# Kernel optimization log

Measured on AMD Instinct MI355X. Metric: run time of the kernel, lower is better.

The kernel has to match this reference:

```python
import jax, jax.numpy as jnp
import numpy as np

N_NODES = 30000
NEG_SLOPE = 0.2  # PyG GATConv default leaky_relu slope


def gat_conv(x, src, dst, W, a_src, a_dst, b, num_nodes, concat):
    """One PyG-style GATConv layer (add_self_loops already applied to src/dst).
    x: [N, F_in]; W: [F_in, H*C]; a_src, a_dst: [H, C]; b: [H*C] or [C].
    """
    H, C = a_src.shape
    h = (x @ W).reshape(num_nodes, H, C)                     # [N, H, C]
    alpha_src = jnp.einsum('nhc,hc->nh', h, a_src)           # [N, H]
    alpha_dst = jnp.einsum('nhc,hc->nh', h, a_dst)           # [N, H]
    e = jax.nn.leaky_relu(alpha_src[src] + alpha_dst[dst], NEG_SLOPE)  # [E, H]
    # scatter-softmax over incoming edges of each dst node
    e_max = jax.ops.segment_max(e, dst, num_segments=num_nodes)        # [N, H]
    e_exp = jnp.exp(e - e_max[dst])                                    # [E, H]
    denom = jax.ops.segment_sum(e_exp, dst, num_segments=num_nodes)    # [N, H]
    alpha = e_exp / denom[dst]                                         # [E, H]
    msg = h[src] * alpha[:, :, None]                                   # [E, H, C]
    out = jax.ops.segment_sum(msg, dst, num_segments=num_nodes)        # [N, H, C]
    out = out.reshape(num_nodes, H * C) if concat else out.mean(axis=1)
    return out + b


def _glorot(key, shape):
    fan = sum(shape[:2]) if len(shape) > 1 else shape[0] * 2
    return jax.random.normal(key, shape, dtype=jnp.float32) * np.sqrt(2.0 / fan)


def setup_inputs() -> dict:
    key = jax.random.key(0)
    ks = jax.random.split(key, 16)
    n, f_in, heads = N_NODES, 256, 4
    x = jax.random.normal(ks[0], (n, f_in), dtype=jnp.float32)
    edge_index = jax.random.randint(ks[1], (2, 480000), 0, n, dtype=jnp.int64)
    inp = {
        'x': x, 'edge_index': edge_index,
        'W1': _glorot(ks[2], (f_in, heads * 128)),
        'a1s': _glorot(ks[3], (heads, 128)), 'a1d': _glorot(ks[4], (heads, 128)),
        'b1': jnp.zeros((heads * 128,), jnp.float32),
        'W2': _glorot(ks[5], (heads * 128, heads * 128)),
        'a2s': _glorot(ks[6], (heads, 128)), 'a2d': _glorot(ks[7], (heads, 128)),
        'b2': jnp.zeros((heads * 128,), jnp.float32),
        'W3': _glorot(ks[8], (heads * 128, heads * 64)),
        'a3s': _glorot(ks[9], (heads, 64)), 'a3d': _glorot(ks[10], (heads, 64)),
        'b3': jnp.zeros((heads * 64,), jnp.float32),
        # conv4: 256 -> 64, 1 head, mean (concat=False)
        'W4': _glorot(ks[11], (heads * 64, 64)),
        'a4s': _glorot(ks[12], (1, 64)), 'a4d': _glorot(ks[13], (1, 64)),
        'b4': jnp.zeros((64,), jnp.float32),
    }
    return inp


def reference(x, edge_index, W1, a1s, a1d, b1, W2, a2s, a2d, b2,
              W3, a3s, a3d, b3, W4, a4s, a4d, b4):
    n = x.shape[0]
    # PyG GATConv default add_self_loops=True
    loops = jnp.arange(n, dtype=edge_index.dtype)
    src = jnp.concatenate([edge_index[0], loops])
    dst = jnp.concatenate([edge_index[1], loops])
    h = jax.nn.relu(gat_conv(x, src, dst, W1, a1s, a1d, b1, n, True))
    h = jax.nn.relu(gat_conv(h, src, dst, W2, a2s, a2d, b2, n, True))
    h = jax.nn.relu(gat_conv(h, src, dst, W3, a3s, a3d, b3, n, True))
    h = jax.nn.relu(gat_conv(h, src, dst, W4, a4s, a4d, b4, n, False))
    return h
```

## Files before the change

kernel.cpp:

```cpp
#include <hip/hip_runtime.h>
#include <hip/hip_fp16.h>
#include <math.h>


typedef __attribute__((ext_vector_type(8))) __bf16 bf16x8;
typedef __attribute__((ext_vector_type(4))) float floatx4;
typedef __attribute__((ext_vector_type(8))) unsigned short usv8;
typedef __attribute__((ext_vector_type(4))) unsigned short usv4;

#define DEG_CAP 256

__device__ __forceinline__ unsigned short f2bf(float f) {
    unsigned int u = __float_as_uint(f);
    u += 0x7fff + ((u >> 16) & 1);
    return (unsigned short)(u >> 16);
}
__device__ __forceinline__ float bf2f(unsigned short u) {
    return __uint_as_float(((unsigned int)u) << 16);
}
__device__ __forceinline__ float lrelu(float e) {
    return (e > 0.f) ? e : 0.2f * e;
}
__device__ __forceinline__ void gload16(const void* g, void* l) {
    __builtin_amdgcn_global_load_lds(
        (const __attribute__((address_space(1))) void*)g,
        (__attribute__((address_space(3))) void*)l, 16, 0, 0);
}

static __global__ void zero_float(float* __restrict__ p, int n) {
    int i = blockIdx.x * blockDim.x + threadIdx.x;
    if (i < n) p[i] = 0.f;
}
static __global__ void zero_int(int* __restrict__ p, int n) {
    int i = blockIdx.x * blockDim.x + threadIdx.x;
    if (i < n) p[i] = 0;
}

static __global__ void hist_kernel(const int* __restrict__ ei, int e0, int n_nodes,
                                   int* __restrict__ counts) {
    int e = blockIdx.x * blockDim.x + threadIdx.x;
    int et = e0 + n_nodes;
    if (e >= et) return;
    int d = (e < e0) ? ei[e0 + e] : (e - e0);
    atomicAdd(&counts[d], 1);
}

static __global__ void scan_kernel(const int* __restrict__ counts,
                                   int* __restrict__ row_ptr,
                                   int* __restrict__ cursor, int n) {
    __shared__ int sdata[1024];
    int tid = threadIdx.x;
    int per = (n + 1023) / 1024;
    int start = tid * per;
    int stop = min(start + per, n);
    if (start > n) start = n;
    int s = 0;
    for (int i = start; i < stop; i++) s += counts[i];
    sdata[tid] = s;
    __syncthreads();
    for (int off = 1; off < 1024; off <<= 1) {
        int t = (tid >= off) ? sdata[tid - off] : 0;
        __syncthreads();
        sdata[tid] += t;
        __syncthreads();
    }
    int run = sdata[tid] - s;
    for (int i = start; i < stop; i++) {
        row_ptr[i] = run;
        cursor[i] = run;
        run += counts[i];
    }
    if (stop == n) row_ptr[n] = run;
}

static __global__ void scatter_kernel(const int* __restrict__ ei, int e0, int n_nodes,
                                      int* __restrict__ cursor,
                                      int* __restrict__ src_sorted) {
    int e = blockIdx.x * blockDim.x + threadIdx.x;
    int et = e0 + n_nodes;
    if (e >= et) return;
    int s, d;
    if (e < e0) { s = ei[e]; d = ei[e0 + e]; } else { s = e - e0; d = s; }
    int pos = atomicAdd(&cursor[d], 1);
    src_sorted[pos] = s;
}

static __global__ void convA_kernel(const float* __restrict__ X,
                                    unsigned short* __restrict__ A, int M, int K) {
    int idx = blockIdx.x * 256 + threadIdx.x;
    if (idx >= M * K) return;
    int m = idx / K, k = idx % K;
    float v = X[idx];
    unsigned short hi = f2bf(v);
    size_t base = (size_t)m * (2 * K);
    A[base + k] = hi;
    A[base + K + k] = f2bf(v - bf2f(hi));
}

__device__ __forceinline__ void convW_one(const float* W, unsigned short* BT,
                                          int idx, int K, int N) {
    int n = idx / K, k = idx % K;
    float v = (n < N) ? W[(size_t)k * N + n] : 0.f;
    unsigned short hi = f2bf(v);
    size_t base = (size_t)n * (2 * K);
    BT[base + k] = hi;
    BT[base + K + k] = f2bf(v - bf2f(hi));
}

static __global__ void convW_all(const float* __restrict__ W1, unsigned short* __restrict__ BT1,
                                 const float* __restrict__ W2, unsigned short* __restrict__ BT2,
                                 const float* __restrict__ W3, unsigned short* __restrict__ BT3,
                                 const float* __restrict__ W4, unsigned short* __restrict__ BT4) {
    int idx = blockIdx.x * 256 + threadIdx.x;
    if (idx < 131072) { convW_one(W1, BT1, idx, 256, 512); return; }
    idx -= 131072;
    if (idx < 262144) { convW_one(W2, BT2, idx, 512, 512); return; }
    idx -= 262144;
    if (idx < 131072) { convW_one(W3, BT3, idx, 512, 256); return; }
    idx -= 131072;
    if (idx < 32768)  { convW_one(W4, BT4, idx, 256, 64); }
}

#define BM 128
#define BN 128
#define BKK 32

__launch_bounds__(256, 3)
static __global__ void gemm_mfma(const unsigned short* __restrict__ A,
                                 const unsigned short* __restrict__ B,
                                 __half* __restrict__ C, int M, int K, int N,
                                 int xcols, int mblocks,
                                 const float* __restrict__ asv,
                                 const float* __restrict__ adv,
                                 float* __restrict__ as_out,
                                 float* __restrict__ ad_out,
                                 int Hh, int Cc) {
    __shared__ __align__(16) unsigned short lds[4 * BM * BKK];
    const int tid  = threadIdx.x;
    const int lane = tid & 63;
    const int wave = tid >> 6;

    const int id = blockIdx.x;
    const int band = id / (8 * xcols);
    const int rem = id - band * 8 * xcols;
    const int band_rows = min(8, mblocks - band * 8);
    const int ry = rem % band_rows;
    const int rx = rem / band_rows;
    const int r0 = (band * 8 + ry) * BM;
    const int c0 = rx * BN;

    const int wm = (wave >> 1) * 64;
    const int wn = (wave & 1) * 64;
    const int q   = lane >> 4;
    const int m16 = lane & 15;

    floatx4 acc[4][4];
#pragma unroll
    for (int i = 0; i < 4; i++)
#pragma unroll
        for (int j = 0; j < 4; j++) acc[i][j] = {0.f, 0.f, 0.f, 0.f};

    const size_t sA = (size_t)(2 * K);
    const size_t sB = (size_t)(2 * K);
    char* ldsb = (char*)lds;

#pragma unroll 1
    for (int k0 = 0; k0 < K; k0 += BKK) {
        __syncthreads();
#pragma unroll
        for (int c = 0; c < 2; c++) {
            int slot = c * 256 + tid;
            int row = slot >> 2;
            int gc  = (slot & 3) ^ ((row >> 1) & 3);
            const unsigned short* Ab = A + (size_t)(r0 + row) * sA + k0 + gc * 8;
            const unsigned short* Bb = B + (size_t)(c0 + row) * sB + k0 + gc * 8;
            gload16(Ab,     ldsb + slot * 16);
            gload16(Ab + K, ldsb + 8192 + slot * 16);
            gload16(Bb,     ldsb + 16384 + slot * 16);
            gload16(Bb + K, ldsb + 24576 + slot * 16);
        }
        __syncthreads();
        bf16x8 ah[4], al[4], bh[4], bl[4];
#pragma unroll
        for (int i = 0; i < 4; i++) {
            int row = wm + i * 16 + m16;
            int ch  = q ^ ((row >> 1) & 3);
            int off = (row * 4 + ch) * 16;
            ah[i] = *(const bf16x8*)(ldsb + off);
            al[i] = *(const bf16x8*)(ldsb + 8192 + off);
        }
#pragma unroll
        for (int j = 0; j < 4; j++) {
            int row = wn + j * 16 + m16;
            int ch  = q ^ ((row >> 1) & 3);
            int off = (row * 4 + ch) * 16;
            bh[j] = *(const bf16x8*)(ldsb + 16384 + off);
            bl[j] = *(const bf16x8*)(ldsb + 24576 + off);
        }
#pragma unroll
        for (int i = 0; i < 4; i++)
#pragma unroll
            for (int j = 0; j < 4; j++) {
                acc[i][j] = __builtin_amdgcn_mfma_f32_16x16x32_bf16(
                    ah[i], bh[j], acc[i][j], 0, 0, 0);
                acc[i][j] = __builtin_amdgcn_mfma_f32_16x16x32_bf16(
                    al[i], bh[j], acc[i][j], 0, 0, 0);
                acc[i][j] = __builtin_amdgcn_mfma_f32_16x16x32_bf16(
                    ah[i], bl[j], acc[i][j], 0, 0, 0);
            }
    }
#pragma unroll
    for (int i = 0; i < 4; i++)
#pragma unroll
        for (int j = 0; j < 4; j++)
#pragma unroll
            for (int r = 0; r < 4; r++) {
                int row = r0 + wm + i * 16 + q * 4 + r;
                int col = c0 + wn + j * 16 + m16;
                if (row < M && col < N)
                    C[(size_t)row * N + col] = __float2half(acc[i][j][r]);
            }
    if (c0 + wn < N) {
        int head = (c0 + wn) / Cc;
#pragma unroll
        for (int i = 0; i < 4; i++)
#pragma unroll
            for (int r = 0; r < 4; r++) {
                float ps = 0.f, pd = 0.f;
#pragma unroll
                for (int j = 0; j < 4; j++) {
                    int c = c0 + wn + j * 16 + m16;
                    float v = acc[i][j][r];
                    ps = fmaf(v, asv[c], ps);
                    pd = fmaf(v, adv[c], pd);
                }
#pragma unroll
                for (int off = 1; off < 16; off <<= 1) {
                    ps += __shfl_xor(ps, off);
                    pd += __shfl_xor(pd, off);
                }
                if (m16 == 0) {
                    int row = r0 + wm + i * 16 + q * 4 + r;
                    if (row < M) {
                        atomicAdd(&as_out[(size_t)row * Hh + head], ps);
                        atomicAdd(&ad_out[(size_t)row * Hh + head], pd);
                    }
                }
            }
    }
}

template <int R>
__device__ __forceinline__ void accum_row(const __half* hptr, size_t off, float w,
                                          float* acc) {
    const __half* p = hptr + off;
    if constexpr (R == 8) {
        float4 raw = *(const float4*)p;
        const __half* hv = (const __half*)&raw;
#pragma unroll
        for (int r = 0; r < 8; r++) acc[r] = fmaf(__half2float(hv[r]), w, acc[r]);
    } else if constexpr (R == 4) {
        float2 raw = *(const float2*)p;
        const __half* hv = (const __half*)&raw;
#pragma unroll
        for (int r = 0; r < 4; r++) acc[r] = fmaf(__half2float(hv[r]), w, acc[r]);
    } else {
        acc[0] = fmaf(__half2float(*p), w, acc[0]);
    }
}

template <int H, int C, bool BF16OUT>
__launch_bounds__(256)
static __global__ void agg_kernel(const __half* __restrict__ h,
                                  const float* __restrict__ as_arr,
                                  const float* __restrict__ ad_arr,
                                  const int* __restrict__ row_ptr,
                                  const int* __restrict__ src_sorted,
                                  const float* __restrict__ bias,
                                  float* __restrict__ outf,
                                  unsigned short* __restrict__ outb,
                                  float* __restrict__ znext_as,
                                  float* __restrict__ znext_ad, int n_nodes) {
    constexpr int R = H * C / 64;
    constexpr int G = 64 / H;
    constexpr int K = H * C;
    __shared__ float lds_e[4][DEG_CAP * H];
    int wave = threadIdx.x >> 6;
    int lane = threadIdx.x & 63;
    int n = blockIdx.x * 4 + wave;
    if (n >= n_nodes) return;
    int beg = row_ptr[n], end = row_ptr[n + 1];
    float* we = lds_e[wave];

    float ad_h[H], m_h[H], l_h[H];
#pragma unroll
    for (int hh = 0; hh < H; hh++) {
        ad_h[hh] = ad_arr[(size_t)n * H + hh];
        m_h[hh] = -INFINITY;
        l_h[hh] = 0.f;
    }
    for (int base = beg; base < end; base += 64) {
        int j = base + lane;
        bool ok = j < end;
        float e_h[H];
        if (ok) {
            int s = src_sorted[j];
            if constexpr (H == 4) {
                float4 a = ((const float4*)as_arr)[s];
                e_h[0] = lrelu(a.x + ad_h[0]);
                e_h[1] = lrelu(a.y + ad_h[1]);
                e_h[2] = lrelu(a.z + ad_h[2]);
                e_h[3] = lrelu(a.w + ad_h[3]);
            } else {
                e_h[0] = lrelu(as_arr[s] + ad_h[0]);
            }
            int idx = j - beg;
            if (idx < DEG_CAP) {
                if constexpr (H == 4) {
                    *(float4*)&we[idx * 4] = make_float4(e_h[0], e_h[1], e_h[2], e_h[3]);
                } else {
                    we[idx] = e_h[0];
                }
            }
        } else {
#pragma unroll
            for (int hh = 0; hh < H; hh++) e_h[hh] = -INFINITY;
        }
#pragma unroll
        for (int hh = 0; hh < H; hh++) {
            float cm = e_h[hh];
#pragma unroll
            for (int off = 1; off < 64; off <<= 1) cm = fmaxf(cm, __shfl_xor(cm, off));
            float newm = fmaxf(m_h[hh], cm);
            float p = ok ? __expf(e_h[hh] - newm) : 0.f;
#pragma unroll
            for (int off = 1; off < 64; off <<= 1) p += __shfl_xor(p, off);
            l_h[hh] = l_h[hh] * __expf(m_h[hh] - newm) + p;
            m_h[hh] = newm;
        }
    }
    int myh = lane / G;
    float mm, adm, inv;
    if constexpr (H == 4) {
        mm  = m_h[0];  mm  = (myh == 1) ? m_h[1] : mm;  mm  = (myh == 2) ? m_h[2] : mm;  mm  = (myh == 3) ? m_h[3] : mm;
        float ll = l_h[0]; ll = (myh == 1) ? l_h[1] : ll; ll = (myh == 2) ? l_h[2] : ll; ll = (myh == 3) ? l_h[3] : ll;
        adm = ad_h[0]; adm = (myh == 1) ? ad_h[1] : adm; adm = (myh == 2) ? ad_h[2] : adm; adm = (myh == 3) ? ad_h[3] : adm;
        inv = 1.f / ll;
    } else {
        mm = m_h[0]; adm = ad_h[0]; inv = 1.f / l_h[0];
    }

    float acc[R];
#pragma unroll
    for (int r = 0; r < R; r++) acc[r] = 0.f;

    int j = beg;
    for (; j + 3 < end; j += 4) {
        int i0 = j - beg;
        int s0 = src_sorted[j];
        int s1 = src_sorted[j + 1];
        int s2 = src_sorted[j + 2];
        int s3 = src_sorted[j + 3];
        float e0, e1, e2, e3;
        if (i0 + 3 < DEG_CAP) {
            e0 = we[(i0 + 0) * H + myh];
            e1 = we[(i0 + 1) * H + myh];
            e2 = we[(i0 + 2) * H + myh];
            e3 = we[(i0 + 3) * H + myh];
        } else {
            e0 = lrelu(as_arr[(size_t)s0 * H + myh] + adm);
            e1 = lrelu(as_arr[(size_t)s1 * H + myh] + adm);
            e2 = lrelu(as_arr[(size_t)s2 * H + myh] + adm);
            e3 = lrelu(as_arr[(size_t)s3 * H + myh] + adm);
        }
        float w0 = __expf(e0 - mm) * inv;
        float w1 = __expf(e1 - mm) * inv;
        float w2 = __expf(e2 - mm) * inv;
        float w3 = __expf(e3 - mm) * inv;
        accum_row<R>(h, (size_t)s0 * K + lane * R, w0, acc);
        accum_row<R>(h, (size_t)s1 * K + lane * R, w1, acc);
        accum_row<R>(h, (size_t)s2 * K + lane * R, w2, acc);
        accum_row<R>(h, (size_t)s3 * K + lane * R, w3, acc);
    }
    for (; j < end; j++) {
        int i0 = j - beg;
        int s0 = src_sorted[j];
        float e0 = (i0 < DEG_CAP) ? we[i0 * H + myh]
                                  : lrelu(as_arr[(size_t)s0 * H + myh] + adm);
        float w0 = __expf(e0 - mm) * inv;
        accum_row<R>(h, (size_t)s0 * K + lane * R, w0, acc);
    }

    if (znext_as != nullptr && lane == 0) {
        if constexpr (H == 4) {
            *(float4*)&znext_as[(size_t)n * 4] = make_float4(0.f, 0.f, 0.f, 0.f);
            *(float4*)&znext_ad[(size_t)n * 4] = make_float4(0.f, 0.f, 0.f, 0.f);
        } else {
            znext_as[n] = 0.f;
            znext_ad[n] = 0.f;
        }
    }
    float vout[R];
#pragma unroll
    for (int r = 0; r < R; r++)
        vout[r] = fmaxf(acc[r] + bias[lane * R + r], 0.f);

    if constexpr (BF16OUT) {
        unsigned short hi[R], lo[R];
#pragma unroll
        for (int r = 0; r < R; r++) {
            hi[r] = f2bf(vout[r]);
            lo[r] = f2bf(vout[r] - bf2f(hi[r]));
        }
        size_t base = (size_t)n * (2 * K) + lane * R;
        if constexpr (R == 8) {
            usv8 vh = {hi[0], hi[1], hi[2], hi[3], hi[4], hi[5], hi[6], hi[7]};
            usv8 vl = {lo[0], lo[1], lo[2], lo[3], lo[4], lo[5], lo[6], lo[7]};
            *(usv8*)(outb + base) = vh;
            *(usv8*)(outb + base + K) = vl;
        } else if constexpr (R == 4) {
            usv4 vh = {hi[0], hi[1], hi[2], hi[3]};
            usv4 vl = {lo[0], lo[1], lo[2], lo[3]};
            *(usv4*)(outb + base) = vh;
            *(usv4*)(outb + base + K) = vl;
        } else {
#pragma unroll
            for (int r = 0; r < R; r++) {
                outb[base + r] = hi[r];
                outb[base + K + r] = lo[r];
            }
        }
    } else {
#pragma unroll
        for (int r = 0; r < R; r++)
            outf[(size_t)n * K + lane * R + r] = vout[r];
    }
}


static inline size_t align_up(size_t x) { return (x + 255) & ~(size_t)255; }

extern "C" void kernel_launch(void* const* d_in, const int* in_sizes, int n_in,
                              void* d_out, int out_size, void* d_ws, size_t ws_size,
                              hipStream_t stream) {
    const float* x   = (const float*)d_in[0];
    const int*   ei  = (const int*)d_in[1];
    const float* W1  = (const float*)d_in[2];
    const float* a1s = (const float*)d_in[3];
    const float* a1d = (const float*)d_in[4];
    const float* b1  = (const float*)d_in[5];
    const float* W2  = (const float*)d_in[6];
    const float* a2s = (const float*)d_in[7];
    const float* a2d = (const float*)d_in[8];
    const float* b2  = (const float*)d_in[9];
    const float* W3  = (const float*)d_in[10];
    const float* a3s = (const float*)d_in[11];
    const float* a3d = (const float*)d_in[12];
    const float* b3  = (const float*)d_in[13];
    const float* W4  = (const float*)d_in[14];
    const float* a4s = (const float*)d_in[15];
    const float* a4d = (const float*)d_in[16];
    const float* b4  = (const float*)d_in[17];

    const int n  = in_sizes[0] / 256;
    const int e0 = in_sizes[1] / 2;
    const int et = e0 + n;
    const int Mpad = ((n + 127) / 128) * 128;

    char* w = (char*)d_ws;
    unsigned short* slotA = (unsigned short*)w;  w += align_up((size_t)Mpad * 1024 * 2);
    __half* hbuf = (__half*)w;                   w += align_up((size_t)n * 512 * 4);
    unsigned short* WT1 = (unsigned short*)w;    w += align_up((size_t)512 * 512 * 2);
    unsigned short* WT2 = (unsigned short*)w;    w += align_up((size_t)512 * 1024 * 2);
    unsigned short* WT3 = (unsigned short*)w;    w += align_up((size_t)256 * 1024 * 2);
    unsigned short* WT4 = (unsigned short*)w;    w += align_up((size_t)128 * 512 * 2);
    float* asA = (float*)w;                      w += align_up((size_t)n * 4 * 4);
    float* adA = (float*)w;                      w += align_up((size_t)n * 4 * 4);
    float* asB = (float*)w;                      w += align_up((size_t)n * 4 * 4);
    float* adB = (float*)w;                      w += align_up((size_t)n * 4 * 4);
    int* row_ptr = (int*)w;                      w += align_up((size_t)(n + 1) * 4);
    int* counts  = (int*)w;                      w += align_up((size_t)n * 4);
    int* cursor  = (int*)w;                      w += align_up((size_t)n * 4);
    int* src_sorted = (int*)w;                   w += align_up((size_t)et * 4);
    (void)ws_size;

    dim3 blk(256);
    int nodeblocks = (n + 3) / 4;

    zero_int<<<(n + 255) / 256, 256, 0, stream>>>(counts, n);
    hist_kernel<<<(et + 255) / 256, 256, 0, stream>>>(ei, e0, n, counts);
    scan_kernel<<<1, 1024, 0, stream>>>(counts, row_ptr, cursor, n);
    scatter_kernel<<<(et + 255) / 256, 256, 0, stream>>>(ei, e0, n, cursor, src_sorted);

    convA_kernel<<<((n * 256) + 255) / 256, blk, 0, stream>>>(x, slotA, n, 256);
    convW_all<<<(557056 + 255) / 256, blk, 0, stream>>>(W1, WT1, W2, WT2, W3, WT3, W4, WT4);
    zero_float<<<(n * 8 + 255) / 256, blk, 0, stream>>>(asA, n * 8);

    const int mblocks = Mpad / 128;

    gemm_mfma<<<dim3(4 * mblocks), blk, 0, stream>>>(slotA, WT1, hbuf, n, 256, 512, 4, mblocks,
                                                     a1s, a1d, asA, adA, 4, 128);
    agg_kernel<4, 128, true><<<nodeblocks, blk, 0, stream>>>(hbuf, asA, adA, row_ptr, src_sorted, b1, nullptr, slotA, asB, adB, n);

    gemm_mfma<<<dim3(4 * mblocks), blk, 0, stream>>>(slotA, WT2, hbuf, n, 512, 512, 4, mblocks,
                                                     a2s, a2d, asB, adB, 4, 128);
    agg_kernel<4, 128, true><<<nodeblocks, blk, 0, stream>>>(hbuf, asB, adB, row_ptr, src_sorted, b2, nullptr, slotA, asA, adA, n);

    gemm_mfma<<<dim3(2 * mblocks), blk, 0, stream>>>(slotA, WT3, hbuf, n, 512, 256, 2, mblocks,
                                                     a3s, a3d, asA, adA, 4, 64);
    agg_kernel<4, 64, true><<<nodeblocks, blk, 0, stream>>>(hbuf, asA, adA, row_ptr, src_sorted, b3, nullptr, slotA, asB, adB, n);

    gemm_mfma<<<dim3(1 * mblocks), blk, 0, stream>>>(slotA, WT4, hbuf, n, 256, 64, 1, mblocks,
                                                     a4s, a4d, asB, adB, 1, 64);
    agg_kernel<1, 64, false><<<nodeblocks, blk, 0, stream>>>(hbuf, asB, adB, row_ptr, src_sorted, b4, (float*)d_out, nullptr, nullptr, nullptr, n);
}
```

Measured before the change: 639.6 us.

## Switch GEMM operands from split-bf16 to fp16 activations with split-fp16 weights

Activations are now stored as a single fp16 value instead of a bf16 hi/lo pair, and weights as an fp16 hi/lo pair. Each tile product therefore needs two MFMA calls instead of three, and the activation loads, LDS footprint and aggregation output writes are halved. Activations are double-buffered in separate fp16 buffers. The risk is lower accuracy: fp16 activations carry about 11 bits of mantissa and have limited range, where split bf16 carried about 16 bits.

```diff
diff --git a/kernel.cpp b/kernel.cpp
--- a/kernel.cpp
+++ b/kernel.cpp
@@ -3,21 +3,13 @@
 #include <math.h>
 
 
-typedef __attribute__((ext_vector_type(8))) __bf16 bf16x8;
+typedef __attribute__((ext_vector_type(8))) _Float16 f16x8;
 typedef __attribute__((ext_vector_type(4))) float floatx4;
 typedef __attribute__((ext_vector_type(8))) unsigned short usv8;
 typedef __attribute__((ext_vector_type(4))) unsigned short usv4;
 
 #define DEG_CAP 256
 
-__device__ __forceinline__ unsigned short f2bf(float f) {
-    unsigned int u = __float_as_uint(f);
-    u += 0x7fff + ((u >> 16) & 1);
-    return (unsigned short)(u >> 16);
-}
-__device__ __forceinline__ float bf2f(unsigned short u) {
-    return __uint_as_float(((unsigned int)u) << 16);
-}
 __device__ __forceinline__ float lrelu(float e) {
     return (e > 0.f) ? e : 0.2f * e;
 }
@@ -86,31 +78,27 @@
 }
 
 static __global__ void convA_kernel(const float* __restrict__ X,
-                                    unsigned short* __restrict__ A, int M, int K) {
+                                    __half* __restrict__ A, int total) {
     int idx = blockIdx.x * 256 + threadIdx.x;
-    if (idx >= M * K) return;
-    int m = idx / K, k = idx % K;
-    float v = X[idx];
-    unsigned short hi = f2bf(v);
-    size_t base = (size_t)m * (2 * K);
-    A[base + k] = hi;
-    A[base + K + k] = f2bf(v - bf2f(hi));
-}
-
-__device__ __forceinline__ void convW_one(const float* W, unsigned short* BT,
+    if (idx >= total) return;
+    A[idx] = __float2half(X[idx]);
+}
+
+__device__ __forceinline__ void convW_one(const float* W, __half* BT,
                                           int idx, int K, int N) {
     int n = idx / K, k = idx % K;
     float v = (n < N) ? W[(size_t)k * N + n] : 0.f;
-    unsigned short hi = f2bf(v);
+    __half hi = __float2half(v);
+    __half lo = __float2half(v - __half2float(hi));
     size_t base = (size_t)n * (2 * K);
     BT[base + k] = hi;
-    BT[base + K + k] = f2bf(v - bf2f(hi));
-}
-
-static __global__ void convW_all(const float* __restrict__ W1, unsigned short* __restrict__ BT1,
-                                 const float* __restrict__ W2, unsigned short* __restrict__ BT2,
-                                 const float* __restrict__ W3, unsigned short* __restrict__ BT3,
-                                 const float* __restrict__ W4, unsigned short* __restrict__ BT4) {
+    BT[base + K + k] = lo;
+}
+
+static __global__ void convW_all(const float* __restrict__ W1, __half* __restrict__ BT1,
+                                 const float* __restrict__ W2, __half* __restrict__ BT2,
+                                 const float* __restrict__ W3, __half* __restrict__ BT3,
+                                 const float* __restrict__ W4, __half* __restrict__ BT4) {
     int idx = blockIdx.x * 256 + threadIdx.x;
     if (idx < 131072) { convW_one(W1, BT1, idx, 256, 512); return; }
     idx -= 131072;
@@ -126,8 +114,8 @@
 #define BKK 32
 
 __launch_bounds__(256, 3)
-static __global__ void gemm_mfma(const unsigned short* __restrict__ A,
-                                 const unsigned short* __restrict__ B,
+static __global__ void gemm_mfma(const __half* __restrict__ A,
+                                 const __half* __restrict__ B,
                                  __half* __restrict__ C, int M, int K, int N,
                                  int xcols, int mblocks,
                                  const float* __restrict__ asv,
@@ -135,7 +123,7 @@
                                  float* __restrict__ as_out,
                                  float* __restrict__ ad_out,
                                  int Hh, int Cc) {
-    __shared__ __align__(16) unsigned short lds[4 * BM * BKK];
+    __shared__ __align__(16) __half lds[3 * BM * BKK];
     const int tid  = threadIdx.x;
     const int lane = tid & 63;
     const int wave = tid >> 6;
@@ -160,7 +148,6 @@
 #pragma unroll
         for (int j = 0; j < 4; j++) acc[i][j] = {0.f, 0.f, 0.f, 0.f};
 
-    const size_t sA = (size_t)(2 * K);
     const size_t sB = (size_t)(2 * K);
     char* ldsb = (char*)lds;
 
@@ -172,41 +159,36 @@
             int slot = c * 256 + tid;
             int row = slot >> 2;
             int gc  = (slot & 3) ^ ((row >> 1) & 3);
-            const unsigned short* Ab = A + (size_t)(r0 + row) * sA + k0 + gc * 8;
-            const unsigned short* Bb = B + (size_t)(c0 + row) * sB + k0 + gc * 8;
-            gload16(Ab,     ldsb + slot * 16);
-            gload16(Ab + K, ldsb + 8192 + slot * 16);
-            gload16(Bb,     ldsb + 16384 + slot * 16);
-            gload16(Bb + K, ldsb + 24576 + slot * 16);
+            gload16(A + (size_t)(r0 + row) * K + k0 + gc * 8,
+                    ldsb + slot * 16);
+            const __half* Bb = B + (size_t)(c0 + row) * sB + k0 + gc * 8;
+            gload16(Bb,     ldsb + 8192 + slot * 16);
+            gload16(Bb + K, ldsb + 16384 + slot * 16);
         }
         __syncthreads();
-        bf16x8 ah[4], al[4], bh[4], bl[4];
+        f16x8 af[4], bh[4], bl[4];
 #pragma unroll
         for (int i = 0; i < 4; i++) {
             int row = wm + i * 16 + m16;
             int ch  = q ^ ((row >> 1) & 3);
-            int off = (row * 4 + ch) * 16;
-            ah[i] = *(const bf16x8*)(ldsb + off);
-            al[i] = *(const bf16x8*)(ldsb + 8192 + off);
+            af[i] = *(const f16x8*)(ldsb + (row * 4 + ch) * 16);
         }
 #pragma unroll
         for (int j = 0; j < 4; j++) {
             int row = wn + j * 16 + m16;
             int ch  = q ^ ((row >> 1) & 3);
             int off = (row * 4 + ch) * 16;
-            bh[j] = *(const bf16x8*)(ldsb + 16384 + off);
-            bl[j] = *(const bf16x8*)(ldsb + 24576 + off);
+            bh[j] = *(const f16x8*)(ldsb + 8192 + off);
+            bl[j] = *(const f16x8*)(ldsb + 16384 + off);
         }
 #pragma unroll
         for (int i = 0; i < 4; i++)
 #pragma unroll
             for (int j = 0; j < 4; j++) {
-                acc[i][j] = __builtin_amdgcn_mfma_f32_16x16x32_bf16(
-                    ah[i], bh[j], acc[i][j], 0, 0, 0);
-                acc[i][j] = __builtin_amdgcn_mfma_f32_16x16x32_bf16(
-                    al[i], bh[j], acc[i][j], 0, 0, 0);
-                acc[i][j] = __builtin_amdgcn_mfma_f32_16x16x32_bf16(
-                    ah[i], bl[j], acc[i][j], 0, 0, 0);
+                acc[i][j] = __builtin_amdgcn_mfma_f32_16x16x32_f16(
+                    af[i], bh[j], acc[i][j], 0, 0, 0);
+                acc[i][j] = __builtin_amdgcn_mfma_f32_16x16x32_f16(
+                    af[i], bl[j], acc[i][j], 0, 0, 0);
             }
     }
 #pragma unroll
@@ -269,7 +251,7 @@
     }
 }
 
-template <int H, int C, bool BF16OUT>
+template <int H, int C, bool F16OUT>
 __launch_bounds__(256)
 static __global__ void agg_kernel(const __half* __restrict__ h,
                                   const float* __restrict__ as_arr,
@@ -278,7 +260,7 @@
                                   const int* __restrict__ src_sorted,
                                   const float* __restrict__ bias,
                                   float* __restrict__ outf,
-                                  unsigned short* __restrict__ outb,
+                                  __half* __restrict__ outh,
                                   float* __restrict__ znext_as,
                                   float* __restrict__ znext_ad, int n_nodes) {
     constexpr int R = H * C / 64;
@@ -405,30 +387,21 @@
     for (int r = 0; r < R; r++)
         vout[r] = fmaxf(acc[r] + bias[lane * R + r], 0.f);
 
-    if constexpr (BF16OUT) {
-        unsigned short hi[R], lo[R];
-#pragma unroll
-        for (int r = 0; r < R; r++) {
-            hi[r] = f2bf(vout[r]);
-            lo[r] = f2bf(vout[r] - bf2f(hi[r]));
-        }
-        size_t base = (size_t)n * (2 * K) + lane * R;
+    if constexpr (F16OUT) {
+        unsigned short hv[R];
+#pragma unroll
+        for (int r = 0; r < R; r++)
+            hv[r] = __half_as_ushort(__float2half(vout[r]));
+        size_t base = (size_t)n * K + lane * R;
         if constexpr (R == 8) {
-            usv8 vh = {hi[0], hi[1], hi[2], hi[3], hi[4], hi[5], hi[6], hi[7]};
-            usv8 vl = {lo[0], lo[1], lo[2], lo[3], lo[4], lo[5], lo[6], lo[7]};
-            *(usv8*)(outb + base) = vh;
-            *(usv8*)(outb + base + K) = vl;
+            usv8 v = {hv[0], hv[1], hv[2], hv[3], hv[4], hv[5], hv[6], hv[7]};
+            *(usv8*)((unsigned short*)outh + base) = v;
         } else if constexpr (R == 4) {
-            usv4 vh = {hi[0], hi[1], hi[2], hi[3]};
-            usv4 vl = {lo[0], lo[1], lo[2], lo[3]};
-            *(usv4*)(outb + base) = vh;
-            *(usv4*)(outb + base + K) = vl;
+            usv4 v = {hv[0], hv[1], hv[2], hv[3]};
+            *(usv4*)((unsigned short*)outh + base) = v;
         } else {
 #pragma unroll
-            for (int r = 0; r < R; r++) {
-                outb[base + r] = hi[r];
-                outb[base + K + r] = lo[r];
-            }
+            for (int r = 0; r < R; r++) ((unsigned short*)outh)[base + r] = hv[r];
         }
     } else {
 #pragma unroll
@@ -468,12 +441,13 @@
     const int Mpad = ((n + 127) / 128) * 128;
 
     char* w = (char*)d_ws;
-    unsigned short* slotA = (unsigned short*)w;  w += align_up((size_t)Mpad * 1024 * 2);
-    __half* hbuf = (__half*)w;                   w += align_up((size_t)n * 512 * 4);
-    unsigned short* WT1 = (unsigned short*)w;    w += align_up((size_t)512 * 512 * 2);
-    unsigned short* WT2 = (unsigned short*)w;    w += align_up((size_t)512 * 1024 * 2);
-    unsigned short* WT3 = (unsigned short*)w;    w += align_up((size_t)256 * 1024 * 2);
-    unsigned short* WT4 = (unsigned short*)w;    w += align_up((size_t)128 * 512 * 2);
+    __half* bufA = (__half*)w;                   w += align_up((size_t)Mpad * 512 * 2);
+    __half* bufB = (__half*)w;                   w += align_up((size_t)Mpad * 512 * 2);
+    __half* hbuf = (__half*)w;                   w += align_up((size_t)Mpad * 512 * 2);
+    __half* WT1 = (__half*)w;                    w += align_up((size_t)512 * 512 * 2);
+    __half* WT2 = (__half*)w;                    w += align_up((size_t)512 * 1024 * 2);
+    __half* WT3 = (__half*)w;                    w += align_up((size_t)256 * 1024 * 2);
+    __half* WT4 = (__half*)w;                    w += align_up((size_t)128 * 512 * 2);
     float* asA = (float*)w;                      w += align_up((size_t)n * 4 * 4);
     float* adA = (float*)w;                      w += align_up((size_t)n * 4 * 4);
     float* asB = (float*)w;                      w += align_up((size_t)n * 4 * 4);
@@ -492,25 +466,25 @@
     scan_kernel<<<1, 1024, 0, stream>>>(counts, row_ptr, cursor, n);
     scatter_kernel<<<(et + 255) / 256, 256, 0, stream>>>(ei, e0, n, cursor, src_sorted);
 
-    convA_kernel<<<((n * 256) + 255) / 256, blk, 0, stream>>>(x, slotA, n, 256);
+    convA_kernel<<<((n * 256) + 255) / 256, blk, 0, stream>>>(x, bufA, n * 256);
     convW_all<<<(557056 + 255) / 256, blk, 0, stream>>>(W1, WT1, W2, WT2, W3, WT3, W4, WT4);
     zero_float<<<(n * 8 + 255) / 256, blk, 0, stream>>>(asA, n * 8);
 
     const int mblocks = Mpad / 128;
 
-    gemm_mfma<<<dim3(4 * mblocks), blk, 0, stream>>>(slotA, WT1, hbuf, n, 256, 512, 4, mblocks,
+    gemm_mfma<<<dim3(4 * mblocks), blk, 0, stream>>>(bufA, WT1, hbuf, n, 256, 512, 4, mblocks,
                                                      a1s, a1d, asA, adA, 4, 128);
-    agg_kernel<4, 128, true><<<nodeblocks, blk, 0, stream>>>(hbuf, asA, adA, row_ptr, src_sorted, b1, nullptr, slotA, asB, adB, n);
-
-    gemm_mfma<<<dim3(4 * mblocks), blk, 0, stream>>>(slotA, WT2, hbuf, n, 512, 512, 4, mblocks,
+    agg_kernel<4, 128, true><<<nodeblocks, blk, 0, stream>>>(hbuf, asA, adA, row_ptr, src_sorted, b1, nullptr, bufB, asB, adB, n);
+
+    gemm_mfma<<<dim3(4 * mblocks), blk, 0, stream>>>(bufB, WT2, hbuf, n, 512, 512, 4, mblocks,
                                                      a2s, a2d, asB, adB, 4, 128);
-    agg_kernel<4, 128, true><<<nodeblocks, blk, 0, stream>>>(hbuf, asB, adB, row_ptr, src_sorted, b2, nullptr, slotA, asA, adA, n);
-
-    gemm_mfma<<<dim3(2 * mblocks), blk, 0, stream>>>(slotA, WT3, hbuf, n, 512, 256, 2, mblocks,
+    agg_kernel<4, 128, true><<<nodeblocks, blk, 0, stream>>>(hbuf, asB, adB, row_ptr, src_sorted, b2, nullptr, bufA, asA, adA, n);
+
+    gemm_mfma<<<dim3(2 * mblocks), blk, 0, stream>>>(bufA, WT3, hbuf, n, 512, 256, 2, mblocks,
                                                      a3s, a3d, asA, adA, 4, 64);
-    agg_kernel<4, 64, true><<<nodeblocks, blk, 0, stream>>>(hbuf, asA, adA, row_ptr, src_sorted, b3, nullptr, slotA, asB, adB, n);
-
-    gemm_mfma<<<dim3(1 * mblocks), blk, 0, stream>>>(slotA, WT4, hbuf, n, 256, 64, 1, mblocks,
+    agg_kernel<4, 64, true><<<nodeblocks, blk, 0, stream>>>(hbuf, asA, adA, row_ptr, src_sorted, b3, nullptr, bufB, asB, adB, n);
+
+    gemm_mfma<<<dim3(1 * mblocks), blk, 0, stream>>>(bufB, WT4, hbuf, n, 256, 64, 1, mblocks,
                                                      a4s, a4d, asB, adB, 1, 64);
     agg_kernel<1, 64, false><<<nodeblocks, blk, 0, stream>>>(hbuf, asB, adB, row_ptr, src_sorted, b4, (float*)d_out, nullptr, nullptr, nullptr, n);
 }
```

Result: faster. 594.8 us (-7.0%).
